# Kernel optimization log

Hardware: AMD Instinct MI355X
Metric: run time of the kernel (lower is better)

The kernel has to match this reference:

```python
import jax, jax.numpy as jnp
import numpy as np

KERNELS = [(1, 2), (2, 1), (1, 3), (3, 1), (1, 4), (4, 1), (2, 2)]
IN_C, OUT_C = 16, 64
FC_IN, FC_H1, FC_H2, NUM_ACTIONS = 3648, 512, 128, 4


def setup_inputs() -> dict:
    key = jax.random.key(0)
    ks = jax.random.split(key, 32)
    B = 32768
    inp = {"x": jax.random.normal(ks[0], (B, IN_C, 4, 4), dtype=jnp.float32)}
    # conv params, OIHW layout, scaled like torch default init (~1/sqrt(fan_in))
    for i, (kh, kw) in enumerate(KERNELS):
        fan_in = IN_C * kh * kw
        s = 1.0 / np.sqrt(fan_in)
        inp[f"w{i}"] = jax.random.uniform(ks[1 + 2 * i], (OUT_C, IN_C, kh, kw), jnp.float32, -s, s)
        inp[f"b{i}"] = jax.random.uniform(ks[2 + 2 * i], (OUT_C,), jnp.float32, -s, s)
    dims = [(FC_IN, FC_H1), (FC_H1, FC_H2), (FC_H2, NUM_ACTIONS)]
    for j, (din, dout) in enumerate(dims):
        s = 1.0 / np.sqrt(din)
        inp[f"fw{j}"] = jax.random.uniform(ks[15 + 2 * j], (dout, din), jnp.float32, -s, s)
        inp[f"fb{j}"] = jax.random.uniform(ks[16 + 2 * j], (dout,), jnp.float32, -s, s)
    return inp


def _conv_relu_flat(x, w, b):
    # x: [B,16,4,4] NCHW, w: [64,16,kh,kw] OIHW -> flatten to [B, 64*oh*ow]
    y = jax.lax.conv_general_dilated(
        x, w, window_strides=(1, 1), padding="VALID",
        dimension_numbers=("NCHW", "OIHW", "NCHW"))
    y = jax.nn.relu(y + b[None, :, None, None])
    return y.reshape(y.shape[0], -1)


def reference(x, w0, b0, w1, b1, w2, b2, w3, b3, w4, b4, w5, b5, w6, b6,
              fw0, fb0, fw1, fb1, fw2, fb2):
    x = x.reshape(-1, 16, 4, 4).astype(jnp.float32)
    ws = [w0, w1, w2, w3, w4, w5, w6]
    bs = [b0, b1, b2, b3, b4, b5, b6]
    combined = jnp.concatenate(
        [_conv_relu_flat(x, w, b) for w, b in zip(ws, bs)], axis=1)  # [B, 3648]
    h = jax.nn.relu(combined @ fw0.T + fb0)
    h = jax.nn.relu(h @ fw1.T + fb1)
    return h @ fw2.T + fb2
```

## Files before the change

### kernel.cpp

```cpp
#include <hip/hip_runtime.h>
#include <hip/hip_bf16.h>
#include <stdint.h>

typedef __attribute__((ext_vector_type(8))) short s8v;
typedef __attribute__((ext_vector_type(4))) float f32x4;

__device__ __forceinline__ unsigned short f2bf(float f) {
  unsigned u = __builtin_bit_cast(unsigned, f);
  u += 0x7fffu + ((u >> 16) & 1u);
  return (unsigned short)(u >> 16);
}

__device__ __forceinline__ void gl16(const void* g, void* l) {
  __builtin_amdgcn_global_load_lds(
      (const __attribute__((address_space(1))) unsigned int*)g,
      (__attribute__((address_space(3))) unsigned int*)l,
      16, 0, 0);
}


__global__ void cast_bf16_k(const float* __restrict__ s, unsigned short* __restrict__ d, int n4) {
  int i = blockIdx.x * blockDim.x + threadIdx.x;
  if (i < n4) {
    float4 v = reinterpret_cast<const float4*>(s)[i];
    ushort4 o;
    o.x = f2bf(v.x); o.y = f2bf(v.y); o.z = f2bf(v.z); o.w = f2bf(v.w);
    reinterpret_cast<ushort4*>(d)[i] = o;
  }
}

__global__ void prep_conv(
    const float* w0, const float* w1, const float* w2, const float* w3,
    const float* w4, const float* w5, const float* w6,
    const float* b0, const float* b1, const float* b2, const float* b3,
    const float* b4, const float* b5, const float* b6,
    unsigned short* __restrict__ Mt, float* __restrict__ cbias)
{
  int n = blockIdx.x * blockDim.x + threadIdx.x;
  if (n >= 3712) return;
  unsigned short* row = Mt + n * 256;
  for (int i = 0; i < 256; ++i) row[i] = 0;
  if (n >= 3648) { cbias[n] = 0.f; return; }
  const int khs[7] = {1,2,1,3,1,4,2};
  const int kws[7] = {2,1,3,1,4,1,2};
  const int cs[8]  = {0,768,1536,2048,2560,2816,3072,3648};
  const float* ws[7] = {w0,w1,w2,w3,w4,w5,w6};
  const float* bs[7] = {b0,b1,b2,b3,b4,b5,b6};
  int k = 6;
  while (n < cs[k]) --k;
  const int kh = khs[k], kw = kws[k];
  const int ow = 5 - kw, np = (5 - kh) * ow;
  const int r = n - cs[k];
  const int och = r / np, p = r % np;
  const int oi = p / ow, oj = p % ow;
  const float* w = ws[k];
  cbias[n] = bs[k][och];
  for (int c = 0; c < 16; ++c)
    for (int dh = 0; dh < kh; ++dh)
      for (int dw = 0; dw < kw; ++dw)
        row[c * 16 + (oi + dh) * 4 + (oj + dw)] =
            f2bf(w[((och * 16 + c) * kh + dh) * kw + dw]);
}

__global__ void prep_fw0(const float* __restrict__ fw0, unsigned short* __restrict__ outp) {
  int idx = blockIdx.x * 256 + threadIdx.x;
  int nrow = idx / 3712;
  int k = idx - nrow * 3712;
  outp[idx] = (k < 3648) ? f2bf(fw0[nrow * 3648 + k]) : (unsigned short)0;
}

__global__ __launch_bounds__(256) void gemm_bt_relu(
    const unsigned short* __restrict__ A, int lda,
    const unsigned short* __restrict__ Bt, int ldb,
    const float* __restrict__ bias,
    unsigned short* __restrict__ C, int ldc,
    int K, int ntn)
{
  __shared__ unsigned short As[128 * 64];
  __shared__ unsigned short Bs[128 * 64];
  const int tid = threadIdx.x;
  const int lane = tid & 63;
  const int wave = tid >> 6;
  const int wm = wave >> 1, wn = wave & 1;

  const int nwg = gridDim.x;
  const int xcd = blockIdx.x & 7;
  const int idx = blockIdx.x >> 3;
  const int q = nwg >> 3, r = nwg & 7;
  const int wgid = (xcd < r ? xcd * (q + 1) : r * (q + 1) + (xcd - r) * q) + idx;
  const int mt = wgid / ntn;
  const int nt = wgid - mt * ntn;
  const int m0 = mt * 128, n0 = nt * 128;

  f32x4 acc[4][4] = {};

  const unsigned short* Ag = A + (size_t)(m0 + (lane >> 3)) * lda + (lane & 7) * 8;
  const unsigned short* Bg = Bt + (size_t)(n0 + (lane >> 3)) * ldb + (lane & 7) * 8;
  char* Asb = (char*)As + wave * 4096 + lane * 16;
  char* Bsb = (char*)Bs + wave * 4096 + lane * 16;

  for (int k0 = 0; k0 < K; k0 += 64) {
#pragma unroll
    for (int i = 0; i < 4; ++i) {
      const int inst = wave * 4 + i;
      gl16(Ag + (size_t)(inst * 8) * lda + k0, Asb + i * 1024);
      gl16(Bg + (size_t)(inst * 8) * ldb + k0, Bsb + i * 1024);
    }
    __syncthreads();
    const int arow = wm * 64 + (lane & 15);
    const int brow = wn * 64 + (lane & 15);
    const int kc = (lane >> 4) * 8;
    s8v af[4][2], bfv[4][2];
#pragma unroll
    for (int mi = 0; mi < 4; ++mi)
#pragma unroll
      for (int kk = 0; kk < 2; ++kk)
        af[mi][kk] = *(const s8v*)(As + (arow + mi * 16) * 64 + kk * 32 + kc);
#pragma unroll
    for (int ni = 0; ni < 4; ++ni)
#pragma unroll
      for (int kk = 0; kk < 2; ++kk)
        bfv[ni][kk] = *(const s8v*)(Bs + (brow + ni * 16) * 64 + kk * 32 + kc);
#pragma unroll
    for (int kk = 0; kk < 2; ++kk)
#pragma unroll
      for (int mi = 0; mi < 4; ++mi)
#pragma unroll
        for (int ni = 0; ni < 4; ++ni)
          acc[mi][ni] = __builtin_amdgcn_mfma_f32_16x16x32_bf16(
              af[mi][kk], bfv[ni][kk], acc[mi][ni], 0, 0, 0);
    __syncthreads();
  }

#pragma unroll
  for (int ni = 0; ni < 4; ++ni) {
    const int col = n0 + wn * 64 + ni * 16 + (lane & 15);
    const float bv = bias[col];
#pragma unroll
    for (int mi = 0; mi < 4; ++mi) {
      const int row = m0 + wm * 64 + mi * 16 + (lane >> 4) * 4;
#pragma unroll
      for (int r2 = 0; r2 < 4; ++r2) {
        float v = acc[mi][ni][r2] + bv;
        v = v > 0.f ? v : 0.f;
        C[(size_t)(row + r2) * ldc + col] = f2bf(v);
      }
    }
  }
}

__global__ __launch_bounds__(256) void fc23(
    const unsigned short* __restrict__ h1,
    const unsigned short* __restrict__ fw1b,
    const float* __restrict__ fb1,
    const float* __restrict__ fw2,
    const float* __restrict__ fb2,
    float* __restrict__ out)
{
  __shared__ unsigned short As[64 * 64];
  __shared__ unsigned short Bs[128 * 64];
  __shared__ float h2[64][129];
  const int tid = threadIdx.x;
  const int lane = tid & 63;
  const int wave = tid >> 6;
  const int wm = wave >> 1, wn = wave & 1;
  const int m0 = blockIdx.x * 64;

  f32x4 acc[2][4] = {};

  const unsigned short* Ag = h1 + (size_t)(m0 + (lane >> 3)) * 512 + (lane & 7) * 8;
  const unsigned short* Bg = fw1b + (size_t)(lane >> 3) * 512 + (lane & 7) * 8;
  char* Asb = (char*)As + wave * 2048 + lane * 16;
  char* Bsb = (char*)Bs + wave * 4096 + lane * 16;

  for (int k0 = 0; k0 < 512; k0 += 64) {
#pragma unroll
    for (int i = 0; i < 2; ++i)
      gl16(Ag + (size_t)((wave * 2 + i) * 8) * 512 + k0, Asb + i * 1024);
#pragma unroll
    for (int i = 0; i < 4; ++i)
      gl16(Bg + (size_t)((wave * 4 + i) * 8) * 512 + k0, Bsb + i * 1024);
    __syncthreads();
    const int arow = wm * 32 + (lane & 15);
    const int brow = wn * 64 + (lane & 15);
    const int kc = (lane >> 4) * 8;
    s8v af[2][2], bfv[4][2];
#pragma unroll
    for (int mi = 0; mi < 2; ++mi)
#pragma unroll
      for (int kk = 0; kk < 2; ++kk)
        af[mi][kk] = *(const s8v*)(As + (arow + mi * 16) * 64 + kk * 32 + kc);
#pragma unroll
    for (int ni = 0; ni < 4; ++ni)
#pragma unroll
      for (int kk = 0; kk < 2; ++kk)
        bfv[ni][kk] = *(const s8v*)(Bs + (brow + ni * 16) * 64 + kk * 32 + kc);
#pragma unroll
    for (int kk = 0; kk < 2; ++kk)
#pragma unroll
      for (int mi = 0; mi < 2; ++mi)
#pragma unroll
        for (int ni = 0; ni < 4; ++ni)
          acc[mi][ni] = __builtin_amdgcn_mfma_f32_16x16x32_bf16(
              af[mi][kk], bfv[ni][kk], acc[mi][ni], 0, 0, 0);
    __syncthreads();
  }

#pragma unroll
  for (int ni = 0; ni < 4; ++ni) {
    const int col = wn * 64 + ni * 16 + (lane & 15);
    const float bv = fb1[col];
#pragma unroll
    for (int mi = 0; mi < 2; ++mi) {
      const int rl = wm * 32 + mi * 16 + (lane >> 4) * 4;
#pragma unroll
      for (int r = 0; r < 4; ++r) {
        float v = acc[mi][ni][r] + bv;
        h2[rl + r][col] = v > 0.f ? v : 0.f;
      }
    }
  }
  __syncthreads();

  const int r = tid >> 2, j = tid & 3;
  const float* w = fw2 + j * 128;
  float dot = fb2[j];
#pragma unroll 8
  for (int c = 0; c < 128; ++c) dot += h2[r][c] * w[c];
  out[(size_t)(m0 + r) * 4 + j] = dot;
}


extern "C" void kernel_launch(void* const* d_in, const int* in_sizes, int n_in,
                              void* d_out, int out_size, void* d_ws, size_t ws_size,
                              hipStream_t stream) {
  const float* x = (const float*)d_in[0];
  const float* w[7];
  const float* b[7];
  for (int i = 0; i < 7; ++i) {
    w[i] = (const float*)d_in[1 + 2 * i];
    b[i] = (const float*)d_in[2 + 2 * i];
  }
  const float* fw0 = (const float*)d_in[15];
  const float* fb0 = (const float*)d_in[16];
  const float* fw1 = (const float*)d_in[17];
  const float* fb1 = (const float*)d_in[18];
  const float* fw2 = (const float*)d_in[19];
  const float* fb2 = (const float*)d_in[20];

  auto a256 = [](size_t v) { return (v + 255) & ~(size_t)255; };
  const size_t persistent =
      a256((size_t)3712 * 256 * 2) +
      a256((size_t)3712 * 4) +
      a256((size_t)512 * 3712 * 2) +
      a256((size_t)128 * 512 * 2);

  int CH = 0;
  for (int c = 32768; c >= 128; c >>= 1) {
    size_t need = persistent + a256((size_t)c * 256 * 2)
                             + a256((size_t)c * 3712 * 2)
                             + a256((size_t)c * 512 * 2);
    if (need <= ws_size) { CH = c; break; }
  }
  if (!CH) return;

  char* ws = (char*)d_ws;
  size_t off = 0;
  auto alloc = [&](size_t bytes) {
    void* p = ws + off;
    off += (bytes + 255) & ~(size_t)255;
    return p;
  };
  unsigned short* Mt   = (unsigned short*)alloc((size_t)3712 * 256 * 2);
  float*          cb   = (float*)alloc((size_t)3712 * 4);
  unsigned short* fw0b = (unsigned short*)alloc((size_t)512 * 3712 * 2);
  unsigned short* fw1b = (unsigned short*)alloc((size_t)128 * 512 * 2);
  unsigned short* xb   = (unsigned short*)alloc((size_t)CH * 256 * 2);
  unsigned short* comb = (unsigned short*)alloc((size_t)CH * 3712 * 2);
  unsigned short* h1   = (unsigned short*)alloc((size_t)CH * 512 * 2);

  cast_bf16_k<<<64, 256, 0, stream>>>(fw1, fw1b, 16384);
  prep_conv<<<15, 256, 0, stream>>>(w[0], w[1], w[2], w[3], w[4], w[5], w[6],
                                    b[0], b[1], b[2], b[3], b[4], b[5], b[6], Mt, cb);
  prep_fw0<<<7424, 256, 0, stream>>>(fw0, fw0b);

  const int nchunks = 32768 / CH;
  const int mtiles = CH / 128;
  for (int c = 0; c < nchunks; ++c) {
    const size_t row0 = (size_t)c * CH;
    cast_bf16_k<<<(CH * 64 + 255) / 256, 256, 0, stream>>>(
        x + row0 * 256, xb, CH * 64);
    gemm_bt_relu<<<mtiles * 29, 256, 0, stream>>>(
        xb, 256, Mt, 256, cb, comb, 3712, 256, 29);
    gemm_bt_relu<<<mtiles * 4, 256, 0, stream>>>(
        comb, 3712, fw0b, 3712, fb0, h1, 512, 3712, 4);
    fc23<<<CH / 64, 256, 0, stream>>>(
        h1, fw1b, fb1, fw2, fb2, (float*)d_out + row0 * 4);
  }
}
```

Baseline: 487.4 us.

## Fuse conv GEMM with fc1 GEMM to keep combined activations on-chip

Replaces the two separate GEMM launches (conv-as-GEMM writing the 3712-wide combined tensor to global memory, then fc1 reading it back) with one kernel. Each 512-thread block owns 128 batch rows, keeps their bf16 input in LDS, and walks the 29 conv column tiles. For each tile it computes the ReLU'd conv output into a swizzled LDS buffer and immediately accumulates it into the 512-wide fc1 result. The chunking loop is removed, so the input cast and fc2/fc3 run once over the whole batch. This removes the large intermediate round-trip through HBM and several launches. In exchange, fc1 weights are streamed straight from global/L2 by every block without LDS staging, and the large LDS footprint plus the big accumulator array limit occupancy to about one block per CU.

```diff
diff --git a/kernel.cpp b/kernel.cpp
--- a/kernel.cpp
+++ b/kernel.cpp
@@ -69,81 +69,136 @@
   outp[idx] = (k < 3648) ? f2bf(fw0[nrow * 3648 + k]) : (unsigned short)0;
 }
 
-__global__ __launch_bounds__(256) void gemm_bt_relu(
-    const unsigned short* __restrict__ A, int lda,
-    const unsigned short* __restrict__ Bt, int ldb,
-    const float* __restrict__ bias,
-    unsigned short* __restrict__ C, int ldc,
-    int K, int ntn)
+__global__ __launch_bounds__(512, 2) void fused_conv_fc1(
+    const unsigned short* __restrict__ xb,
+    const unsigned short* __restrict__ Mt,
+    const float* __restrict__ cbias,
+    const unsigned short* __restrict__ fw0b,
+    const float* __restrict__ fb0,
+    unsigned short* __restrict__ h1)
 {
-  __shared__ unsigned short As[128 * 64];
-  __shared__ unsigned short Bs[128 * 64];
+  __shared__ unsigned short xs[128 * 256];
+  __shared__ unsigned short ms[128 * 128];
+  __shared__ unsigned short ps[128 * 128];
   const int tid = threadIdx.x;
   const int lane = tid & 63;
-  const int wave = tid >> 6;
-  const int wm = wave >> 1, wn = wave & 1;
-
-  const int nwg = gridDim.x;
-  const int xcd = blockIdx.x & 7;
-  const int idx = blockIdx.x >> 3;
-  const int q = nwg >> 3, r = nwg & 7;
-  const int wgid = (xcd < r ? xcd * (q + 1) : r * (q + 1) + (xcd - r) * q) + idx;
-  const int mt = wgid / ntn;
-  const int nt = wgid - mt * ntn;
-  const int m0 = mt * 128, n0 = nt * 128;
-
-  f32x4 acc[4][4] = {};
-
-  const unsigned short* Ag = A + (size_t)(m0 + (lane >> 3)) * lda + (lane & 7) * 8;
-  const unsigned short* Bg = Bt + (size_t)(n0 + (lane >> 3)) * ldb + (lane & 7) * 8;
-  char* Asb = (char*)As + wave * 4096 + lane * 16;
-  char* Bsb = (char*)Bs + wave * 4096 + lane * 16;
-
-  for (int k0 = 0; k0 < K; k0 += 64) {
-#pragma unroll
-    for (int i = 0; i < 4; ++i) {
-      const int inst = wave * 4 + i;
-      gl16(Ag + (size_t)(inst * 8) * lda + k0, Asb + i * 1024);
-      gl16(Bg + (size_t)(inst * 8) * ldb + k0, Bsb + i * 1024);
+  const int w = tid >> 6;
+  const int wm = w >> 2;
+  const int wn = w & 3;
+  const int g8 = lane >> 4;
+  const int l15 = lane & 15;
+  const int m0 = blockIdx.x * 128;
+
+  {
+    char* dst = (char*)xs + (w * 8) * 1024 + lane * 16;
+#pragma unroll
+    for (int i = 0; i < 8; ++i) {
+      int c = (w * 8 + i) * 64 + lane;
+      int row = c >> 5, col16 = c & 31;
+      int cs = col16 ^ (row & 7);
+      gl16(xb + (size_t)(m0 + row) * 256 + cs * 8, dst + i * 1024);
+    }
+  }
+
+  f32x4 acc[4][8] = {};
+
+#pragma unroll 1
+  for (int j = 0; j < 29; ++j) {
+    f32x4 accp[4][2] = {};
+    const int ar = wm * 64 + l15;
+    const int br = wn * 32 + l15;
+#pragma unroll 1
+    for (int h = 0; h < 2; ++h) {
+      __syncthreads();
+      {
+        char* dst = (char*)ms + (w * 4) * 1024 + lane * 16;
+#pragma unroll
+        for (int i = 0; i < 4; ++i) {
+          int c = (w * 4 + i) * 64 + lane;
+          int row = c >> 4, col16 = c & 15;
+          int cs = col16 ^ (row & 7);
+          gl16(Mt + (size_t)(j * 128 + row) * 256 + h * 128 + cs * 8, dst + i * 1024);
+        }
+      }
+      __syncthreads();
+#pragma unroll
+      for (int kk = 0; kk < 4; ++kk) {
+        const int cx = h * 16 + kk * 4 + g8;
+        const int cm = kk * 4 + g8;
+        s8v xa[4], mb[2];
+#pragma unroll
+        for (int mi = 0; mi < 4; ++mi) {
+          int r = ar + mi * 16;
+          xa[mi] = *(const s8v*)((const char*)xs + r * 512 + ((cx ^ (r & 7)) << 4));
+        }
+#pragma unroll
+        for (int ni = 0; ni < 2; ++ni) {
+          int r = br + ni * 16;
+          mb[ni] = *(const s8v*)((const char*)ms + r * 256 + ((cm ^ (r & 7)) << 4));
+        }
+#pragma unroll
+        for (int mi = 0; mi < 4; ++mi)
+#pragma unroll
+          for (int ni = 0; ni < 2; ++ni)
+            accp[mi][ni] = __builtin_amdgcn_mfma_f32_16x16x32_bf16(
+                xa[mi], mb[ni], accp[mi][ni], 0, 0, 0);
+      }
+    }
+#pragma unroll
+    for (int ni = 0; ni < 2; ++ni) {
+      const int pc = wn * 32 + ni * 16 + l15;
+      const float bv = cbias[j * 128 + pc];
+#pragma unroll
+      for (int mi = 0; mi < 4; ++mi) {
+#pragma unroll
+        for (int r = 0; r < 4; ++r) {
+          const int pr = wm * 64 + mi * 16 + g8 * 4 + r;
+          float v = accp[mi][ni][r] + bv;
+          v = v > 0.f ? v : 0.f;
+          *(unsigned short*)((char*)ps + pr * 256 +
+                             (((pc >> 3) ^ (pr & 7)) << 4) + (pc & 7) * 2) = f2bf(v);
+        }
+      }
     }
     __syncthreads();
-    const int arow = wm * 64 + (lane & 15);
-    const int brow = wn * 64 + (lane & 15);
-    const int kc = (lane >> 4) * 8;
-    s8v af[4][2], bfv[4][2];
-#pragma unroll
-    for (int mi = 0; mi < 4; ++mi)
-#pragma unroll
-      for (int kk = 0; kk < 2; ++kk)
-        af[mi][kk] = *(const s8v*)(As + (arow + mi * 16) * 64 + kk * 32 + kc);
-#pragma unroll
-    for (int ni = 0; ni < 4; ++ni)
-#pragma unroll
-      for (int kk = 0; kk < 2; ++kk)
-        bfv[ni][kk] = *(const s8v*)(Bs + (brow + ni * 16) * 64 + kk * 32 + kc);
-#pragma unroll
-    for (int kk = 0; kk < 2; ++kk)
+
+    const int kbase = j * 128;
+#pragma unroll
+    for (int kk = 0; kk < 4; ++kk) {
+      const int c16 = kk * 4 + g8;
+      s8v pa[4], fwb[8];
+#pragma unroll
+      for (int mi = 0; mi < 4; ++mi) {
+        int r = wm * 64 + mi * 16 + l15;
+        pa[mi] = *(const s8v*)((const char*)ps + r * 256 + ((c16 ^ (r & 7)) << 4));
+      }
+      const int kf = kbase + kk * 32 + g8 * 8;
+#pragma unroll
+      for (int ni = 0; ni < 8; ++ni) {
+        int bn = wn * 128 + ni * 16 + l15;
+        fwb[ni] = *(const s8v*)(fw0b + (size_t)bn * 3712 + kf);
+      }
 #pragma unroll
       for (int mi = 0; mi < 4; ++mi)
 #pragma unroll
-        for (int ni = 0; ni < 4; ++ni)
+        for (int ni = 0; ni < 8; ++ni)
           acc[mi][ni] = __builtin_amdgcn_mfma_f32_16x16x32_bf16(
-              af[mi][kk], bfv[ni][kk], acc[mi][ni], 0, 0, 0);
-    __syncthreads();
-  }
-
-#pragma unroll
-  for (int ni = 0; ni < 4; ++ni) {
-    const int col = n0 + wn * 64 + ni * 16 + (lane & 15);
-    const float bv = bias[col];
+              pa[mi], fwb[ni], acc[mi][ni], 0, 0, 0);
+    }
+  }
+
+#pragma unroll
+  for (int ni = 0; ni < 8; ++ni) {
+    const int col = wn * 128 + ni * 16 + l15;
+    const float bv = fb0[col];
 #pragma unroll
     for (int mi = 0; mi < 4; ++mi) {
-      const int row = m0 + wm * 64 + mi * 16 + (lane >> 4) * 4;
-#pragma unroll
-      for (int r2 = 0; r2 < 4; ++r2) {
-        float v = acc[mi][ni][r2] + bv;
+      const int row = m0 + wm * 64 + mi * 16 + g8 * 4;
+#pragma unroll
+      for (int r = 0; r < 4; ++r) {
+        float v = acc[mi][ni][r] + bv;
         v = v > 0.f ? v : 0.f;
-        C[(size_t)(row + r2) * ldc + col] = f2bf(v);
+        h1[(size_t)(row + r) * 512 + col] = f2bf(v);
       }
     }
   }
@@ -248,22 +303,6 @@
   const float* fw2 = (const float*)d_in[19];
   const float* fb2 = (const float*)d_in[20];
 
-  auto a256 = [](size_t v) { return (v + 255) & ~(size_t)255; };
-  const size_t persistent =
-      a256((size_t)3712 * 256 * 2) +
-      a256((size_t)3712 * 4) +
-      a256((size_t)512 * 3712 * 2) +
-      a256((size_t)128 * 512 * 2);
-
-  int CH = 0;
-  for (int c = 32768; c >= 128; c >>= 1) {
-    size_t need = persistent + a256((size_t)c * 256 * 2)
-                             + a256((size_t)c * 3712 * 2)
-                             + a256((size_t)c * 512 * 2);
-    if (need <= ws_size) { CH = c; break; }
-  }
-  if (!CH) return;
-
   char* ws = (char*)d_ws;
   size_t off = 0;
   auto alloc = [&](size_t bytes) {
@@ -275,26 +314,16 @@
   float*          cb   = (float*)alloc((size_t)3712 * 4);
   unsigned short* fw0b = (unsigned short*)alloc((size_t)512 * 3712 * 2);
   unsigned short* fw1b = (unsigned short*)alloc((size_t)128 * 512 * 2);
-  unsigned short* xb   = (unsigned short*)alloc((size_t)CH * 256 * 2);
-  unsigned short* comb = (unsigned short*)alloc((size_t)CH * 3712 * 2);
-  unsigned short* h1   = (unsigned short*)alloc((size_t)CH * 512 * 2);
-
+  unsigned short* xb   = (unsigned short*)alloc((size_t)32768 * 256 * 2);
+  unsigned short* h1   = (unsigned short*)alloc((size_t)32768 * 512 * 2);
+  if (ws_size < off) return;
+
+  cast_bf16_k<<<8192, 256, 0, stream>>>(x, xb, 2097152);
   cast_bf16_k<<<64, 256, 0, stream>>>(fw1, fw1b, 16384);
   prep_conv<<<15, 256, 0, stream>>>(w[0], w[1], w[2], w[3], w[4], w[5], w[6],
                                     b[0], b[1], b[2], b[3], b[4], b[5], b[6], Mt, cb);
   prep_fw0<<<7424, 256, 0, stream>>>(fw0, fw0b);
 
-  const int nchunks = 32768 / CH;
-  const int mtiles = CH / 128;
-  for (int c = 0; c < nchunks; ++c) {
-    const size_t row0 = (size_t)c * CH;
-    cast_bf16_k<<<(CH * 64 + 255) / 256, 256, 0, stream>>>(
-        x + row0 * 256, xb, CH * 64);
-    gemm_bt_relu<<<mtiles * 29, 256, 0, stream>>>(
-        xb, 256, Mt, 256, cb, comb, 3712, 256, 29);
-    gemm_bt_relu<<<mtiles * 4, 256, 0, stream>>>(
-        comb, 3712, fw0b, 3712, fb0, h1, 512, 3712, 4);
-    fc23<<<CH / 64, 256, 0, stream>>>(
-        h1, fw1b, fb1, fw2, fb2, (float*)d_out + row0 * 4);
-  }
-}
+  fused_conv_fc1<<<256, 512, 0, stream>>>(xb, Mt, cb, fw0b, fb0, h1);
+  fc23<<<512, 256, 0, stream>>>(h1, fw1b, fb1, fw2, fb2, (float*)d_out);
+}
```

Measured after the change: 584.4 us. +19.9%, slower.
